# Performance work log

Hardware: AMD Instinct MI355X
Metric: run time of the kernel (lower is better)

## Reference

```python
import jax, jax.numpy as jnp
import numpy as np


def setup_inputs() -> dict:
    key = jax.random.key(0)
    k1, k2 = jax.random.split(key)
    x = jax.random.normal(k1, (8, 4096, 256), dtype=jnp.float32)
    codebooks = jax.random.normal(k2, (8, 1024, 256), dtype=jnp.float32)
    return {"x": x, "codebooks": codebooks}


def reference(x, codebooks):
    """Residual VQ (eval mode, no quantize dropout).

    x:         [b, n, d] float
    codebooks: [q, c, d] float (one Euclidean codebook per quantizer level)
    Returns (quantized_out [b,n,d], all_indices [b,n,q] int32, all_losses [b,q]).
    """

    def step(carry, embed):
        residual, qout = carry  # each [b, n, d]; embed: [c, d]
        # squared Euclidean distance [b, n, c] (the ||residual||^2 term is
        # constant over c but kept for faithfulness to cdist semantics)
        d2 = (
            jnp.sum(residual * residual, axis=-1, keepdims=True)
            - 2.0 * jnp.einsum("bnd,cd->bnc", residual, embed)
            + jnp.sum(embed * embed, axis=-1)
        )
        idx = jnp.argmin(d2, axis=-1)  # [b, n]
        quantized = embed[idx]  # [b, n, d] gather
        # commitment loss per batch element
        loss = jnp.mean(
            (jax.lax.stop_gradient(quantized) - residual) ** 2, axis=(1, 2)
        )  # [b]
        # straight-through estimator
        q_st = residual + jax.lax.stop_gradient(quantized - residual)
        return (residual - q_st, qout + q_st), (idx.astype(jnp.int32), loss)

    init = (x, jnp.zeros_like(x))
    (_, quantized_out), (indices, losses) = jax.lax.scan(step, init, codebooks)
    all_indices = jnp.moveaxis(indices, 0, -1)  # [b, n, q]
    all_losses = jnp.moveaxis(losses, 0, -1)    # [b, q]
    return quantized_out, all_indices, all_losses
```

## Files before the change

### kernel.cpp

```cpp
#include <hip/hip_runtime.h>
#include <math.h>

#define NB 8
#define NN 4096
#define DD 256
#define CC 1024
#define NQ 8
#define ROWS (NB*NN)
#define TAU 0.0625f

typedef unsigned short u16;
typedef __attribute__((ext_vector_type(8))) _Float16 f16x8;
typedef __attribute__((ext_vector_type(4))) float f32x4;

__device__ __forceinline__ u16 f2h(float f) {
  _Float16 h = (_Float16)f;
  return __builtin_bit_cast(u16, h);
}
__device__ __forceinline__ void hi4h(float4 f, ushort4& h) {
  h.x = f2h(f.x); h.y = f2h(f.y); h.z = f2h(f.z); h.w = f2h(f.w);
}

__device__ __forceinline__ void merge_top2(float& v1, float& c1, float& v2, float& c2,
                                           float w1, float d1, float w2, float d2) {
  if (w1 < v1 || (w1 == v1 && d1 < c1)) {
    float nv2, nc2;
    if (v1 < w2 || (v1 == w2 && c1 < d2)) { nv2 = v1; nc2 = c1; }
    else                                  { nv2 = w2; nc2 = d2; }
    v1 = w1; c1 = d1; v2 = nv2; c2 = nc2;
  } else {
    if (w1 < v2 || (w1 == v2 && d1 < c2)) { v2 = w1; c2 = d1; }
  }
}

__device__ __forceinline__ void gload16(const void* g, void* l) {
  __builtin_amdgcn_global_load_lds(
      (const __attribute__((address_space(1))) unsigned int*)g,
      (__attribute__((address_space(3))) unsigned int*)l, 16, 0, 0);
}

__global__ __launch_bounds__(256) void rvq_split0(
    const float* __restrict__ x, u16* __restrict__ rsplit, int* __restrict__ cnt)
{
  if (blockIdx.x == 0 && threadIdx.x < NQ) cnt[threadIdx.x] = 0;
  const size_t f = (size_t)blockIdx.x * 256 + threadIdx.x;
  const size_t row = f >> 6;
  const int c4 = (int)(f & 63) << 2;
  float4 v = ((const float4*)x)[f];
  ushort4 h; hi4h(v, h);
  *(ushort4*)(rsplit + row * 256 + c4) = h;
}

__global__ __launch_bounds__(256) void rvq_esplit_all(
    const float* __restrict__ cb, u16* __restrict__ esp)
{
  const int f = blockIdx.x * 256 + threadIdx.x;
  const int row = f >> 6;
  const int c4 = (f & 63) << 2;
  float4 v = ((const float4*)cb)[f];
  ushort4 h; hi4h(v, h);
  *(ushort4*)(esp + (size_t)row * 256 + c4) = h;
}

__global__ __launch_bounds__(256) void rvq_norms(
    const float* __restrict__ cb, float* __restrict__ cn2)
{
  const int tid = threadIdx.x;
  const size_t code = (size_t)blockIdx.x * 4 + (tid >> 6);
  const int l = tid & 63;
  const float4 v = *reinterpret_cast<const float4*>(cb + code * DD + l * 4);
  float s = v.x * v.x + v.y * v.y + v.z * v.z + v.w * v.w;
  #pragma unroll
  for (int mm = 1; mm < 64; mm <<= 1) s += __shfl_xor(s, mm);
  if (l == 0) cn2[code] = s;
}

__global__ __launch_bounds__(256) void rvq_gemm97(
    const u16* __restrict__ rsplit,
    const u16* __restrict__ esp,
    const float* __restrict__ cn2q,
    float4* __restrict__ top2)
{
  __shared__ __align__(16) u16 shm[24576];
  #define AS(c) (shm + (c) * 4096)
  #define BS(c) (shm + 12288 + (c) * 4096)

  const int tid = threadIdx.x;
  const int lane = tid & 63;
  const int wv = tid >> 6;
  const int wr = wv >> 1, wc = wv & 1;
  const int fr = lane & 15, fg = lane >> 4;
  const int bid = blockIdx.x;
  const int mb = ((bid >> 6) << 3) | (bid & 7);
  const int nb = (bid >> 3) & 7;
  const size_t row0 = (size_t)mb * 128;

  const int jl = lane ^ ((lane >> 3) & 3);
  const int lrow = jl >> 2;
  const int lc4 = jl & 3;

  const int j = (fr << 2) + fg;
  const int js8 = (j ^ ((j >> 3) & 3)) << 3;

  auto stage = [&](int t, int cur) {
    const int o = (t & 7) << 5;
    #pragma unroll
    for (int r = 0; r < 2; ++r) {
      const int r0 = ((r << 2) + wv) << 4;
      const int grow = r0 + lrow;
      gload16(rsplit + (row0 + grow) * 256 + o + (lc4 << 3), AS(cur) + r0 * 32);
      gload16(esp + (size_t)(nb * 128 + grow) * 256 + o + (lc4 << 3), BS(cur) + r0 * 32);
    }
  };

  f32x4 acc[4][4];
  #pragma unroll
  for (int m = 0; m < 4; ++m)
    #pragma unroll
    for (int n = 0; n < 4; ++n) acc[m][n] = (f32x4){0.f, 0.f, 0.f, 0.f};

  stage(0, 0);
  stage(1, 1);
  __builtin_amdgcn_sched_barrier(0);
  asm volatile("s_waitcnt vmcnt(4)" ::: "memory");
  __builtin_amdgcn_s_barrier();
  __builtin_amdgcn_sched_barrier(0);

  for (int t = 0; t < 8; ++t) {
    const int cur = t % 3;
    if (t + 2 < 8) stage(t + 2, (t + 2) % 3);
    f16x8 a[4], b[4];
    #pragma unroll
    for (int m = 0; m < 4; ++m)
      a[m] = *(const f16x8*)&AS(cur)[(((wr << 2) + m) << 9) + js8];
    #pragma unroll
    for (int n = 0; n < 4; ++n)
      b[n] = *(const f16x8*)&BS(cur)[(((wc << 2) + n) << 9) + js8];
    #pragma unroll
    for (int m = 0; m < 4; ++m)
      #pragma unroll
      for (int n = 0; n < 4; ++n)
        acc[m][n] = __builtin_amdgcn_mfma_f32_16x16x32_f16(a[m], b[n], acc[m][n], 0, 0, 0);
    __builtin_amdgcn_sched_barrier(0);
    if (t < 6) {
      asm volatile("s_waitcnt vmcnt(4)" ::: "memory");
    } else {
      asm volatile("s_waitcnt vmcnt(0)" ::: "memory");
    }
    __builtin_amdgcn_s_barrier();
    __builtin_amdgcn_sched_barrier(0);
  }

  float4* arena = (float4*)shm;
  float cnv[4];
  #pragma unroll
  for (int n = 0; n < 4; ++n) cnv[n] = cn2q[nb * 128 + wc * 64 + n * 16 + fr];

  #pragma unroll
  for (int m = 0; m < 4; ++m)
    #pragma unroll
    for (int r = 0; r < 4; ++r) {
      float v1 = __builtin_inff(), c1 = 1.0e9f, v2 = __builtin_inff(), c2 = 1.0e9f;
      #pragma unroll
      for (int n = 0; n < 4; ++n) {
        const float sv = fmaf(-2.f, acc[m][n][r], cnv[n]);
        const float cf = (float)(nb * 128 + wc * 64 + n * 16 + fr);
        if (sv < v1) { v2 = v1; c2 = c1; v1 = sv; c1 = cf; }
        else if (sv < v2) { v2 = sv; c2 = cf; }
      }
      float w1 = __shfl_xor(v1, 1), d1 = __shfl_xor(c1, 1);
      float w2 = __shfl_xor(v2, 1), d2 = __shfl_xor(c2, 1);
      merge_top2(v1, c1, v2, c2, w1, d1, w2, d2);
      if ((fr & 1) == 0) {
        const int row128 = wr * 64 + m * 16 + fg * 4 + r;
        const int slot = (wc * 8 + (fr >> 1) + row128) & 15;
        arena[row128 * 16 + slot] = make_float4(v1, c1, v2, c2);
      }
    }
  __syncthreads();

  if (tid < 128) {
    float4 g0 = arena[tid * 16 + (tid & 15)];
    float v1 = g0.x, c1 = g0.y, v2 = g0.z, c2 = g0.w;
    #pragma unroll
    for (int s = 1; s < 16; ++s) {
      float4 g = arena[tid * 16 + ((s + tid) & 15)];
      merge_top2(v1, c1, v2, c2, g.x, g.y, g.z, g.w);
    }
    top2[(row0 + tid) * 8 + nb] = make_float4(v1, c1, v2, c2);
  }
  #undef AS
  #undef BS
}

__global__ __launch_bounds__(256) void rvq_reduce(
    const float4* __restrict__ top2, float* __restrict__ idx_out,
    int* __restrict__ list, int* __restrict__ cnt, int level)
{
  const int row = blockIdx.x * 256 + threadIdx.x;
  const float4* p = top2 + (size_t)row * 8;
  float4 f = p[0];
  float v1 = f.x, c1 = f.y, v2 = f.z, c2 = f.w;
  #pragma unroll
  for (int i = 1; i < 8; ++i) {
    float4 g = p[i];
    merge_top2(v1, c1, v2, c2, g.x, g.y, g.z, g.w);
  }
  idx_out[(size_t)row * NQ + level] = c1;
  if (v2 - v1 <= TAU) {
    int q = atomicAdd(cnt + level, 1);
    list[q] = row;
  }
}

__global__ __launch_bounds__(256) void rvq_cleanup(
    const float* __restrict__ src, const float* __restrict__ cbq,
    const float* __restrict__ cn2q, const int* __restrict__ list,
    const int* __restrict__ cnt, float* __restrict__ idx_out, int level)
{
  __shared__ __align__(16) float rsh[DD];
  __shared__ float wmin[4];
  __shared__ int wcol[4];
  const int tid = threadIdx.x;
  const int n = cnt[level];
  for (int it = blockIdx.x; it < n; it += gridDim.x) {
    const int row = list[it];
    __syncthreads();
    rsh[tid] = src[(size_t)row * DD + tid];
    __syncthreads();
    float bv = __builtin_inff(); int bc = 1 << 29;
    #pragma unroll
    for (int cc4 = 0; cc4 < 4; ++cc4) {
      const int c = cc4 * 256 + tid;
      const float4* ep = (const float4*)(cbq + (size_t)c * DD);
      float dot = 0.f;
      #pragma unroll 8
      for (int k4 = 0; k4 < 64; ++k4) {
        float4 e4 = ep[k4];
        float4 r4 = *(const float4*)&rsh[k4 * 4];
        dot = fmaf(r4.x, e4.x, dot);
        dot = fmaf(r4.y, e4.y, dot);
        dot = fmaf(r4.z, e4.z, dot);
        dot = fmaf(r4.w, e4.w, dot);
      }
      float s = fmaf(-2.f, dot, cn2q[c]);
      if (s < bv || (s == bv && c < bc)) { bv = s; bc = c; }
    }
    #pragma unroll
    for (int mk = 1; mk < 64; mk <<= 1) {
      float ov = __shfl_xor(bv, mk); int oc = __shfl_xor(bc, mk);
      if (ov < bv || (ov == bv && oc < bc)) { bv = ov; bc = oc; }
    }
    if ((tid & 63) == 0) { wmin[tid >> 6] = bv; wcol[tid >> 6] = bc; }
    __syncthreads();
    if (tid == 0) {
      float v = wmin[0]; int c = wcol[0];
      #pragma unroll
      for (int w = 1; w < 4; ++w)
        if (wmin[w] < v || (wmin[w] == v && wcol[w] < c)) { v = wmin[w]; c = wcol[w]; }
      idx_out[(size_t)row * NQ + level] = (float)c;
    }
  }
}

__global__ __launch_bounds__(256) void rvq_update_split(
    const float* __restrict__ x, const float* __restrict__ src,
    float* __restrict__ res, const float* __restrict__ cbq,
    const float* __restrict__ idx_f, u16* __restrict__ rsplit,
    float* __restrict__ partials, int level)
{
  const int tid = threadIdx.x;
  const size_t row = (size_t)blockIdx.x * 4 + (tid >> 6);
  const int seg = (tid & 63) << 2;
  const int idx = (int)idx_f[row * NQ + level];
  const float4 e = *reinterpret_cast<const float4*>(cbq + (size_t)idx * DD + seg);
  const float4 r = *reinterpret_cast<const float4*>(src + row * DD + seg);
  float4 rn = make_float4(r.x - e.x, r.y - e.y, r.z - e.z, r.w - e.w);
  if (level < 7) {
    *reinterpret_cast<float4*>(res + row * DD + seg) = rn;
    ushort4 h; hi4h(rn, h);
    *(ushort4*)(rsplit + row * 256 + seg) = h;
  } else {
    const float4 xv = *reinterpret_cast<const float4*>(x + row * DD + seg);
    *reinterpret_cast<float4*>(res + row * DD + seg) =
        make_float4(xv.x - rn.x, xv.y - rn.y, xv.z - rn.z, xv.w - rn.w);
  }
  float p = rn.x * rn.x + rn.y * rn.y + rn.z * rn.z + rn.w * rn.w;
  #pragma unroll
  for (int mm = 1; mm < 64; mm <<= 1) p += __shfl_xor(p, mm);
  __shared__ float w4[4];
  if ((tid & 63) == 0) w4[tid >> 6] = p;
  __syncthreads();
  if (tid == 0) partials[blockIdx.x] = w4[0] + w4[1] + w4[2] + w4[3];
}

__global__ __launch_bounds__(256) void rvq_loss(
    const float* __restrict__ partials, float* __restrict__ loss_out, int level)
{
  const int b = blockIdx.x;
  const int tid = threadIdx.x;
  float s = 0.f;
  for (int i = tid; i < 1024; i += 256) s += partials[b * 1024 + i];
  #pragma unroll
  for (int mm = 1; mm < 64; mm <<= 1) s += __shfl_xor(s, mm);
  __shared__ float w4[4];
  if ((tid & 63) == 0) w4[tid >> 6] = s;
  __syncthreads();
  if (tid == 0)
    loss_out[b * NQ + level] = (w4[0] + w4[1] + w4[2] + w4[3]) * (1.0f / 1048576.0f);
}

extern "C" void kernel_launch(void* const* d_in, const int* in_sizes, int n_in,
                              void* d_out, int out_size, void* d_ws, size_t ws_size,
                              hipStream_t stream) {
  const float* x  = (const float*)d_in[0];
  const float* cb = (const float*)d_in[1];
  float* out = (float*)d_out;

  float* res      = out;
  float* out_idx  = out + (size_t)ROWS * DD;
  float* out_loss = out_idx + (size_t)ROWS * NQ;

  char* w = (char*)d_ws;
  u16* rsplit = (u16*)w;                         w += (size_t)ROWS * 256 * 2;
  u16* esp = (u16*)w;                            w += (size_t)NQ * CC * 256 * 2;
  float4* top2 = (float4*)w;                     w += (size_t)ROWS * 8 * 16;
  int* list = (int*)w;                           w += (size_t)NQ * ROWS * 4;
  float* cn2 = (float*)w;                        w += (size_t)NQ * CC * 4;
  float* partials = (float*)w;                   w += (size_t)(ROWS / 4) * 4;
  int* cnt = (int*)w;                            w += 64;

  rvq_split0<<<8192, 256, 0, stream>>>(x, rsplit, cnt);
  rvq_esplit_all<<<2048, 256, 0, stream>>>(cb, esp);
  rvq_norms<<<2048, 256, 0, stream>>>(cb, cn2);

  for (int q = 0; q < NQ; ++q) {
    const float* srcres = q ? res : x;
    const size_t eo = (size_t)q * CC * DD;
    rvq_gemm97<<<2048, 256, 0, stream>>>(
        rsplit, esp + (size_t)q * CC * 256, cn2 + (size_t)q * CC, top2);
    rvq_reduce<<<128, 256, 0, stream>>>(top2, out_idx, list + (size_t)q * ROWS, cnt, q);
    rvq_cleanup<<<512, 256, 0, stream>>>(
        srcres, cb + eo, cn2 + (size_t)q * CC, list + (size_t)q * ROWS, cnt, out_idx, q);
    rvq_update_split<<<ROWS / 4, 256, 0, stream>>>(
        x, srcres, res, cb + eo, out_idx, rsplit, partials, q);
    rvq_loss<<<NB, 256, 0, stream>>>(partials, out_loss, q);
  }
}
```

Measured before the change: 783.7 us.

## Replace LDS-staged GEMM with register-direct double-buffered loads and 64x64 per-wave tiles

The distance GEMM no longer stages A/B tiles through shared memory with global_load_lds and block barriers. Each wave now loads its fp16 fragments straight from global memory into registers, double-buffered across the eight K steps, and computes its own 64-code column tile. The block tile shrinks to 64 rows, and the per-row top-2 results are now split 16 ways in a column-major layout, so the reduce kernel merges 16 candidates per row instead of 8. This removes LDS traffic and barriers, but it loses the reuse of each A/B tile across waves, so more global and L2 traffic is needed per MFMA.

```diff
diff --git a/kernel.cpp b/kernel.cpp
--- a/kernel.cpp
+++ b/kernel.cpp
@@ -33,12 +33,6 @@
   }
 }
 
-__device__ __forceinline__ void gload16(const void* g, void* l) {
-  __builtin_amdgcn_global_load_lds(
-      (const __attribute__((address_space(1))) unsigned int*)g,
-      (__attribute__((address_space(3))) unsigned int*)l, 16, 0, 0);
-}
-
 __global__ __launch_bounds__(256) void rvq_split0(
     const float* __restrict__ x, u16* __restrict__ rsplit, int* __restrict__ cnt)
 {
@@ -75,43 +69,25 @@
   if (l == 0) cn2[code] = s;
 }
 
-__global__ __launch_bounds__(256) void rvq_gemm97(
+__global__ __launch_bounds__(256) void rvq_gemm_reg(
     const u16* __restrict__ rsplit,
     const u16* __restrict__ esp,
     const float* __restrict__ cn2q,
     float4* __restrict__ top2)
 {
-  __shared__ __align__(16) u16 shm[24576];
-  #define AS(c) (shm + (c) * 4096)
-  #define BS(c) (shm + 12288 + (c) * 4096)
+  __shared__ float4 arena[4][64 * 8];
 
   const int tid = threadIdx.x;
   const int lane = tid & 63;
   const int wv = tid >> 6;
-  const int wr = wv >> 1, wc = wv & 1;
   const int fr = lane & 15, fg = lane >> 4;
   const int bid = blockIdx.x;
-  const int mb = ((bid >> 6) << 3) | (bid & 7);
-  const int nb = (bid >> 3) & 7;
-  const size_t row0 = (size_t)mb * 128;
-
-  const int jl = lane ^ ((lane >> 3) & 3);
-  const int lrow = jl >> 2;
-  const int lc4 = jl & 3;
-
-  const int j = (fr << 2) + fg;
-  const int js8 = (j ^ ((j >> 3) & 3)) << 3;
-
-  auto stage = [&](int t, int cur) {
-    const int o = (t & 7) << 5;
-    #pragma unroll
-    for (int r = 0; r < 2; ++r) {
-      const int r0 = ((r << 2) + wv) << 4;
-      const int grow = r0 + lrow;
-      gload16(rsplit + (row0 + grow) * 256 + o + (lc4 << 3), AS(cur) + r0 * 32);
-      gload16(esp + (size_t)(nb * 128 + grow) * 256 + o + (lc4 << 3), BS(cur) + r0 * 32);
-    }
-  };
+  const int rt = ((bid >> 5) << 3) | (bid & 7);
+  const int ct = (((bid >> 3) & 3) << 2) | wv;
+  const size_t row0 = (size_t)rt * 64;
+
+  const u16* aB = rsplit + (row0 + fr) * 256 + fg * 8;
+  const u16* bB = esp + ((size_t)(ct * 64 + fr)) * 256 + fg * 8;
 
   f32x4 acc[4][4];
   #pragma unroll
@@ -119,42 +95,50 @@
     #pragma unroll
     for (int n = 0; n < 4; ++n) acc[m][n] = (f32x4){0.f, 0.f, 0.f, 0.f};
 
-  stage(0, 0);
-  stage(1, 1);
-  __builtin_amdgcn_sched_barrier(0);
-  asm volatile("s_waitcnt vmcnt(4)" ::: "memory");
-  __builtin_amdgcn_s_barrier();
-  __builtin_amdgcn_sched_barrier(0);
-
-  for (int t = 0; t < 8; ++t) {
-    const int cur = t % 3;
-    if (t + 2 < 8) stage(t + 2, (t + 2) % 3);
-    f16x8 a[4], b[4];
-    #pragma unroll
-    for (int m = 0; m < 4; ++m)
-      a[m] = *(const f16x8*)&AS(cur)[(((wr << 2) + m) << 9) + js8];
-    #pragma unroll
-    for (int n = 0; n < 4; ++n)
-      b[n] = *(const f16x8*)&BS(cur)[(((wc << 2) + n) << 9) + js8];
-    #pragma unroll
-    for (int m = 0; m < 4; ++m)
-      #pragma unroll
-      for (int n = 0; n < 4; ++n)
-        acc[m][n] = __builtin_amdgcn_mfma_f32_16x16x32_f16(a[m], b[n], acc[m][n], 0, 0, 0);
-    __builtin_amdgcn_sched_barrier(0);
-    if (t < 6) {
-      asm volatile("s_waitcnt vmcnt(4)" ::: "memory");
-    } else {
-      asm volatile("s_waitcnt vmcnt(0)" ::: "memory");
-    }
-    __builtin_amdgcn_s_barrier();
-    __builtin_amdgcn_sched_barrier(0);
-  }
-
-  float4* arena = (float4*)shm;
+  f16x8 a0[4], b0[4], a1[4], b1[4];
+
+#define LOADF(adst, bdst, t)                                                  \
+  {                                                                           \
+    _Pragma("unroll")                                                         \
+    for (int m = 0; m < 4; ++m)                                               \
+      adst[m] = *(const f16x8*)(aB + m * 4096 + (t) * 32);                    \
+    _Pragma("unroll")                                                         \
+    for (int n = 0; n < 4; ++n)                                               \
+      bdst[n] = *(const f16x8*)(bB + n * 4096 + (t) * 32);                    \
+  }
+#define MFMAS(a_, b_)                                                         \
+  {                                                                           \
+    _Pragma("unroll")                                                         \
+    for (int m = 0; m < 4; ++m)                                               \
+      _Pragma("unroll")                                                       \
+      for (int n = 0; n < 4; ++n)                                             \
+        acc[m][n] = __builtin_amdgcn_mfma_f32_16x16x32_f16(a_[m], b_[n],      \
+                                                           acc[m][n], 0, 0, 0); \
+  }
+
+  LOADF(a0, b0, 0);
+  LOADF(a1, b1, 1);
+  MFMAS(a0, b0);
+  LOADF(a0, b0, 2);
+  MFMAS(a1, b1);
+  LOADF(a1, b1, 3);
+  MFMAS(a0, b0);
+  LOADF(a0, b0, 4);
+  MFMAS(a1, b1);
+  LOADF(a1, b1, 5);
+  MFMAS(a0, b0);
+  LOADF(a0, b0, 6);
+  MFMAS(a1, b1);
+  LOADF(a1, b1, 7);
+  MFMAS(a0, b0);
+  MFMAS(a1, b1);
+#undef LOADF
+#undef MFMAS
+
   float cnv[4];
   #pragma unroll
-  for (int n = 0; n < 4; ++n) cnv[n] = cn2q[nb * 128 + wc * 64 + n * 16 + fr];
+  for (int n = 0; n < 4; ++n) cnv[n] = cn2q[ct * 64 + n * 16 + fr];
+  float4* my = arena[wv];
 
   #pragma unroll
   for (int m = 0; m < 4; ++m)
@@ -164,7 +148,7 @@
       #pragma unroll
       for (int n = 0; n < 4; ++n) {
         const float sv = fmaf(-2.f, acc[m][n][r], cnv[n]);
-        const float cf = (float)(nb * 128 + wc * 64 + n * 16 + fr);
+        const float cf = (float)(ct * 64 + n * 16 + fr);
         if (sv < v1) { v2 = v1; c2 = c1; v1 = sv; c1 = cf; }
         else if (sv < v2) { v2 = sv; c2 = cf; }
       }
@@ -172,25 +156,24 @@
       float w2 = __shfl_xor(v2, 1), d2 = __shfl_xor(c2, 1);
       merge_top2(v1, c1, v2, c2, w1, d1, w2, d2);
       if ((fr & 1) == 0) {
-        const int row128 = wr * 64 + m * 16 + fg * 4 + r;
-        const int slot = (wc * 8 + (fr >> 1) + row128) & 15;
-        arena[row128 * 16 + slot] = make_float4(v1, c1, v2, c2);
+        const int row64 = m * 16 + fg * 4 + r;
+        my[row64 * 8 + ((fr >> 1) ^ (row64 & 7))] = make_float4(v1, c1, v2, c2);
       }
     }
-  __syncthreads();
-
-  if (tid < 128) {
-    float4 g0 = arena[tid * 16 + (tid & 15)];
+
+  asm volatile("s_waitcnt lgkmcnt(0)" ::: "memory");
+  __builtin_amdgcn_sched_barrier(0);
+  {
+    const int row64 = lane;
+    float4 g0 = my[row64 * 8 + (0 ^ (row64 & 7))];
     float v1 = g0.x, c1 = g0.y, v2 = g0.z, c2 = g0.w;
     #pragma unroll
-    for (int s = 1; s < 16; ++s) {
-      float4 g = arena[tid * 16 + ((s + tid) & 15)];
+    for (int s = 1; s < 8; ++s) {
+      float4 g = my[row64 * 8 + (s ^ (row64 & 7))];
       merge_top2(v1, c1, v2, c2, g.x, g.y, g.z, g.w);
     }
-    top2[(row0 + tid) * 8 + nb] = make_float4(v1, c1, v2, c2);
-  }
-  #undef AS
-  #undef BS
+    top2[(size_t)ct * ROWS + row0 + row64] = make_float4(v1, c1, v2, c2);
+  }
 }
 
 __global__ __launch_bounds__(256) void rvq_reduce(
@@ -198,12 +181,11 @@
     int* __restrict__ list, int* __restrict__ cnt, int level)
 {
   const int row = blockIdx.x * 256 + threadIdx.x;
-  const float4* p = top2 + (size_t)row * 8;
-  float4 f = p[0];
+  float4 f = top2[row];
   float v1 = f.x, c1 = f.y, v2 = f.z, c2 = f.w;
   #pragma unroll
-  for (int i = 1; i < 8; ++i) {
-    float4 g = p[i];
+  for (int i = 1; i < 16; ++i) {
+    float4 g = top2[(size_t)i * ROWS + row];
     merge_top2(v1, c1, v2, c2, g.x, g.y, g.z, g.w);
   }
   idx_out[(size_t)row * NQ + level] = c1;
@@ -324,7 +306,7 @@
   char* w = (char*)d_ws;
   u16* rsplit = (u16*)w;                         w += (size_t)ROWS * 256 * 2;
   u16* esp = (u16*)w;                            w += (size_t)NQ * CC * 256 * 2;
-  float4* top2 = (float4*)w;                     w += (size_t)ROWS * 8 * 16;
+  float4* top2 = (float4*)w;                     w += (size_t)16 * ROWS * 16;
   int* list = (int*)w;                           w += (size_t)NQ * ROWS * 4;
   float* cn2 = (float*)w;                        w += (size_t)NQ * CC * 4;
   float* partials = (float*)w;                   w += (size_t)(ROWS / 4) * 4;
@@ -337,7 +319,7 @@
   for (int q = 0; q < NQ; ++q) {
     const float* srcres = q ? res : x;
     const size_t eo = (size_t)q * CC * DD;
-    rvq_gemm97<<<2048, 256, 0, stream>>>(
+    rvq_gemm_reg<<<2048, 256, 0, stream>>>(
         rsplit, esp + (size_t)q * CC * 256, cn2 + (size_t)q * CC, top2);
     rvq_reduce<<<128, 256, 0, stream>>>(top2, out_idx, list + (size_t)q * ROWS, cnt, q);
     rvq_cleanup<<<512, 256, 0, stream>>>(
```

Measured after the change: 1.172 ms. +49.5%, slower.
